# Kernel tuning notes

Hardware: AMD Instinct MI355X
Metric: run time of the kernel (lower is better)

## Reference

```python
import jax, jax.numpy as jnp
import numpy as np
from jax import lax

HEADS = 8
EPS = 1e-5


def _ln2d(x, g, b):
    # LayerNorm over channel axis of BCHW (torch LayerNorm(dim) after b c h w -> b h w c)
    mu = jnp.mean(x, axis=1, keepdims=True)
    var = jnp.mean(jnp.square(x - mu), axis=1, keepdims=True)
    xn = (x - mu) * lax.rsqrt(var + EPS)
    return xn * g[None, :, None, None] + b[None, :, None, None]


def _conv1x1(x, w, b):
    # w: [out_c, in_c]
    return jnp.einsum('bchw,oc->bohw', x, w) + b[None, :, None, None]


def _dwconv3x3(x, w, b):
    # w: [C, 1, 3, 3], depthwise
    y = lax.conv_general_dilated(x, w, window_strides=(1, 1), padding='SAME',
                                 feature_group_count=x.shape[1],
                                 dimension_numbers=('NCHW', 'OIHW', 'NCHW'))
    return y + b[None, :, None, None]


def _gelu(x):
    return jax.nn.gelu(x, approximate=False)


def _linear_attention(x, qkv_w, qkv_b, out_w, out_b):
    B, C, H, W = x.shape
    hd = C // HEADS
    qkv = _conv1x1(x, qkv_w, qkv_b)              # [B, 3C, H, W]
    q, k, v = jnp.split(qkv, 3, axis=1)
    # b (h c) h0 w0 -> b h c (h0 w0)
    q = q.reshape(B, HEADS, hd, H * W)
    k = k.reshape(B, HEADS, hd, H * W)
    v = v.reshape(B, HEADS, hd, H * W)
    q = jax.nn.softmax(q, axis=2)                # over head_dim
    k = jax.nn.softmax(k, axis=3)                # over pixels
    context = jnp.einsum('bhcn,bhdn->bhcd', k, v)  # [B, H, hd, hd]
    out = jnp.einsum('bhcd,bhcn->bhdn', context, q)  # [B, H, hd, N]
    out = out.reshape(B, C, H, W)
    return _conv1x1(out, out_w, out_b)


def _ffn(x, w1, b1, dw_w, dw_b, w2, b2):
    h = _gelu(_conv1x1(x, w1, b1))
    h = _gelu(_dwconv3x3(h, dw_w, dw_b))
    return _conv1x1(h, w2, b2)


def setup_inputs() -> dict:
    key = jax.random.key(0)
    ks = jax.random.split(key, 6)
    B, C, H, W = 4, 192, 256, 256
    hidden = C * 2
    s = 0.02
    return {
        'x': jax.random.normal(ks[0], (B, C, H, W), jnp.float32),
        'ln1_g': jnp.ones((C,), jnp.float32),
        'ln1_b': jnp.zeros((C,), jnp.float32),
        'qkv_w': jax.random.normal(ks[1], (3 * C, C), jnp.float32) * s,
        'qkv_b': jnp.zeros((3 * C,), jnp.float32),
        'out_w': jax.random.normal(ks[2], (C, C), jnp.float32) * s,
        'out_b': jnp.zeros((C,), jnp.float32),
        'ln2_g': jnp.ones((C,), jnp.float32),
        'ln2_b': jnp.zeros((C,), jnp.float32),
        'w1': jax.random.normal(ks[3], (hidden, C), jnp.float32) * s,
        'b1': jnp.zeros((hidden,), jnp.float32),
        'dw_w': jax.random.normal(ks[4], (hidden, 1, 3, 3), jnp.float32) * s,
        'dw_b': jnp.zeros((hidden,), jnp.float32),
        'w2': jax.random.normal(ks[5], (C, hidden), jnp.float32) * s,
        'b2': jnp.zeros((C,), jnp.float32),
    }


def reference(x, ln1_g, ln1_b, qkv_w, qkv_b, out_w, out_b, ln2_g, ln2_b, w1, b1, dw_w, dw_b, w2, b2):
    x = x + _linear_attention(_ln2d(x, ln1_g, ln1_b), qkv_w, qkv_b, out_w, out_b)
    x = x + _ffn(_ln2d(x, ln2_g, ln2_b), w1, b1, dw_w, dw_b, w2, b2)
    return x
```

## Files before the change

kernel.cpp:

```cpp
#include <hip/hip_runtime.h>
#include <math.h>

typedef __attribute__((ext_vector_type(8))) short s8;
typedef __attribute__((ext_vector_type(8))) unsigned short us8;
typedef __attribute__((ext_vector_type(4))) float f4;
typedef __attribute__((ext_vector_type(4))) unsigned short us4;
typedef __attribute__((ext_vector_type(4))) unsigned int u32x4;

#define DEVI __device__ __forceinline__

static const int NPIX = 65536;

DEVI float b2f(unsigned short u) {
    unsigned int v = ((unsigned int)u) << 16;
    float f; __builtin_memcpy(&f, &v, 4); return f;
}
DEVI unsigned short f2b(float f) {
    unsigned int u; __builtin_memcpy(&u, &f, 4);
    unsigned int r = (u + 0x7FFFu + ((u >> 16) & 1u)) >> 16;
    return (unsigned short)r;
}
DEVI float geluf(float x) { return 0.5f * x * (1.0f + erff(x * 0.70710678118f)); }
DEVI float gelu_t(float x) {
    float z = 1.595769122f * (x + 0.044715f * x * x * x);
    return x * __builtin_amdgcn_rcpf(1.0f + __expf(-z));
}
DEVI float rfl(float v) {
    int i; __builtin_memcpy(&i, &v, 4);
    i = __builtin_amdgcn_readfirstlane(i);
    float o; __builtin_memcpy(&o, &i, 4); return o;
}

DEVI void gload_lds16(const unsigned short* g, unsigned short* l) {
    __builtin_amdgcn_global_load_lds(
        (const __attribute__((address_space(1))) unsigned int*)g,
        (__attribute__((address_space(3))) unsigned int*)l,
        16, 0, 0);
}

__global__ __launch_bounds__(256) void lnt_k(const float* __restrict__ X,
                                             const float* __restrict__ gw,
                                             const float* __restrict__ gb,
                                             unsigned short* __restrict__ Out)
{
    const int i = blockIdx.x * 256 + threadIdx.x;
    const int b = i >> 16, px = i & 65535;
    const float* xp = X + (size_t)b * 192 * NPIX + px;

    unsigned int pk[96];
    float sum = 0.f, ssq = 0.f;
    #pragma unroll
    for (int c = 0; c < 192; c++) {
        float v = xp[(size_t)c * NPIX];
        sum += v; ssq += v * v;
        unsigned int h = f2b(v);
        if (c & 1) pk[c >> 1] |= h << 16;
        else       pk[c >> 1] = h;
    }
    float mu = sum * (1.0f / 192.0f);
    float var = ssq * (1.0f / 192.0f) - mu * mu;
    float rs = rsqrtf(var + 1e-5f);

    #pragma unroll
    for (int c2 = 0; c2 < 96; c2++) {
        int c = c2 * 2;
        float lo = b2f((unsigned short)(pk[c2] & 0xFFFF));
        float hi = b2f((unsigned short)(pk[c2] >> 16));
        lo = (lo - mu) * rs * gw[c] + gb[c];
        hi = (hi - mu) * rs * gw[c + 1] + gb[c + 1];
        pk[c2] = (unsigned int)f2b(lo) | ((unsigned int)f2b(hi) << 16);
    }
    u32x4* dst = (u32x4*)(Out + (size_t)i * 192);
    #pragma unroll
    for (int j = 0; j < 6; j++) {
        u32x4 v = { pk[4 * j], pk[4 * j + 1], pk[4 * j + 2], pk[4 * j + 3] };
        dst[j] = v;
    }
}

template<int MODE, int NCHUNK, int UNITS, int NTILE>
__global__ __launch_bounds__(256) void gemm3_k(
    const unsigned short* __restrict__ X, const unsigned short* __restrict__ Wb,
    const float* __restrict__ bias, const void* __restrict__ resid,
    void* __restrict__ Out, int OCTOT, unsigned short* __restrict__ qT)
{
    constexpr int KTOT = UNITS * 192;
    __shared__ unsigned short tile[2][64 * 192];

    const int tid = threadIdx.x;
    const int wave = tid >> 6, lane = tid & 63;
    const int lr = lane & 15, lg = lane >> 4;
    const int xr = lr & 7;

    auto stage = [&](int s, int buf) {
        const int t = s / UNITS, u = s - t * UNITS;
        const int gp0s = (blockIdx.x * NTILE + t) * 64;
        const unsigned short* Xb = X + (size_t)gp0s * KTOT + u * 192;
        #pragma unroll
        for (int j = 0; j < 6; j++) {
            int ci = (wave * 6 + j) * 64 + lane;
            int row = ci / 24;
            int c = ci - row * 24;
            int csw = (c & ~7) | ((c ^ row) & 7);
            gload_lds16(Xb + (size_t)row * KTOT + csw * 8, &tile[buf][ci * 8]);
        }
    };

    stage(0, 0);

    for (int t = 0; t < NTILE; t++) {
        const int gp0 = (blockIdx.x * NTILE + t) * 64;
        const int b = gp0 >> 16;
        const int pxb = gp0 & 65535;

        if constexpr (UNITS == 1) {
            __syncthreads();
            if (t + 1 < NTILE) stage(t + 1, (t + 1) & 1);
            const unsigned short* tb = tile[t & 1];

            #pragma unroll
            for (int cn = 0; cn < NCHUNK; cn++) {
                const int ocb = cn * 192 + wave * 48;
                const unsigned short* wrow = Wb + (size_t)(ocb + lr) * KTOT + lg * 8;
                const bool swapped = (MODE == 1) || (MODE == 3 && cn == 0);

                s8 wf[3][6];
                #pragma unroll
                for (int ot = 0; ot < 3; ot++)
                    #pragma unroll
                    for (int kk = 0; kk < 6; kk++)
                        wf[ot][kk] = *(const s8*)(wrow + (size_t)ot * 16 * KTOT + kk * 32);

                f4 acc[4][3];
                #pragma unroll
                for (int i = 0; i < 4; i++)
                    #pragma unroll
                    for (int j = 0; j < 3; j++) acc[i][j] = (f4)0.0f;

                #pragma unroll
                for (int kk = 0; kk < 6; kk++) {
                    const int kc = kk * 4 + lg;
                    const int kcs = (kc & ~7) | ((kc ^ xr) & 7);
                    s8 a[4];
                    #pragma unroll
                    for (int pt = 0; pt < 4; pt++)
                        a[pt] = *(const s8*)&tb[((pt * 16 + lr) * 24 + kcs) * 8];
                    #pragma unroll
                    for (int ot = 0; ot < 3; ot++)
                        #pragma unroll
                        for (int pt = 0; pt < 4; pt++)
                            acc[pt][ot] = swapped
                                ? __builtin_amdgcn_mfma_f32_16x16x32_bf16(wf[ot][kk], a[pt], acc[pt][ot], 0, 0, 0)
                                : __builtin_amdgcn_mfma_f32_16x16x32_bf16(a[pt], wf[ot][kk], acc[pt][ot], 0, 0, 0);
                }

                if (MODE == 3 && cn == 0) {
                    #pragma unroll
                    for (int pt = 0; pt < 4; pt++) {
                        const int gp = gp0 + pt * 16 + lr;
                        unsigned short* orow = qT + (size_t)gp * 192 + wave * 48 + lg * 4;
                        #pragma unroll
                        for (int ot = 0; ot < 3; ot++) {
                            f4 bi4 = *(const f4*)&bias[wave * 48 + ot * 16 + lg * 4];
                            us4 o;
                            #pragma unroll
                            for (int r = 0; r < 4; r++) o[r] = f2b(__expf(acc[pt][ot][r] + bi4[r]));
                            *(us4*)(orow + ot * 16) = o;
                        }
                    }
                } else if (MODE == 3) {
                    #pragma unroll
                    for (int ot = 0; ot < 3; ot++) {
                        const int oc = ocb + ot * 16 + lr;
                        const float bi = bias[oc];
                        const size_t rowoff = ((size_t)b * 384 + (oc - 192)) * NPIX + pxb + lg * 4;
                        #pragma unroll
                        for (int pt = 0; pt < 4; pt++) {
                            us4 o;
                            #pragma unroll
                            for (int r = 0; r < 4; r++) {
                                float v = acc[pt][ot][r] + bi;
                                if (cn == 1) v = __expf(v);
                                o[r] = f2b(v);
                            }
                            *(us4*)((unsigned short*)Out + rowoff + pt * 16) = o;
                        }
                    }
                } else {
                    #pragma unroll
                    for (int pt = 0; pt < 4; pt++) {
                        const int gp = gp0 + pt * 16 + lr;
                        unsigned short* orow = (unsigned short*)Out + (size_t)gp * OCTOT + ocb + lg * 4;
                        #pragma unroll
                        for (int ot = 0; ot < 3; ot++) {
                            f4 bi4 = *(const f4*)&bias[ocb + ot * 16 + lg * 4];
                            us4 o;
                            #pragma unroll
                            for (int r = 0; r < 4; r++) o[r] = f2b(geluf(acc[pt][ot][r] + bi4[r]));
                            *(us4*)(orow + ot * 16) = o;
                        }
                    }
                }
            }
        } else {
            const int ocb = wave * 48;
            const unsigned short* wrow = Wb + (size_t)(ocb + lr) * KTOT + lg * 8;

            f4 acc[4][3];
            #pragma unroll
            for (int i = 0; i < 4; i++)
                #pragma unroll
                for (int j = 0; j < 3; j++) acc[i][j] = (f4)0.0f;

            #pragma unroll
            for (int u = 0; u < 2; u++) {
                const int s = t * 2 + u;
                __syncthreads();
                if (s + 1 < NTILE * 2) stage(s + 1, (s + 1) & 1);
                const unsigned short* tb = tile[s & 1];

                s8 wf[3][6];
                #pragma unroll
                for (int ot = 0; ot < 3; ot++)
                    #pragma unroll
                    for (int kk = 0; kk < 6; kk++)
                        wf[ot][kk] = *(const s8*)(wrow + (size_t)ot * 16 * KTOT + u * 192 + kk * 32);

                #pragma unroll
                for (int kk = 0; kk < 6; kk++) {
                    const int kc = kk * 4 + lg;
                    const int kcs = (kc & ~7) | ((kc ^ xr) & 7);
                    s8 a[4];
                    #pragma unroll
                    for (int pt = 0; pt < 4; pt++)
                        a[pt] = *(const s8*)&tb[((pt * 16 + lr) * 24 + kcs) * 8];
                    #pragma unroll
                    for (int ot = 0; ot < 3; ot++)
                        #pragma unroll
                        for (int pt = 0; pt < 4; pt++)
                            acc[pt][ot] = __builtin_amdgcn_mfma_f32_16x16x32_bf16(a[pt], wf[ot][kk], acc[pt][ot], 0, 0, 0);
                }
            }

            #pragma unroll
            for (int ot = 0; ot < 3; ot++) {
                const int oc = ocb + ot * 16 + lr;
                const float bi = bias[oc];
                const size_t rowoff = ((size_t)b * 192 + oc) * NPIX + pxb + lg * 4;
                #pragma unroll
                for (int pt = 0; pt < 4; pt++) {
                    if (MODE == 2) {
                        f4 rv = *(const f4*)((const float*)resid + rowoff + pt * 16);
                        f4 o;
                        #pragma unroll
                        for (int r = 0; r < 4; r++) o[r] = acc[pt][ot][r] + bi + rv[r];
                        *(f4*)((float*)Out + rowoff + pt * 16) = o;
                    } else {
                        us4 rv = *(const us4*)((const unsigned short*)resid + rowoff + pt * 16);
                        f4 o;
                        #pragma unroll
                        for (int r = 0; r < 4; r++) o[r] = acc[pt][ot][r] + bi + b2f(rv[r]);
                        *(f4*)((float*)Out + rowoff + pt * 16) = o;
                    }
                }
            }
        }
    }
}

__global__ void zero_k(float* __restrict__ p, int n)
{
    int i = blockIdx.x * 256 + threadIdx.x;
    if (i < n) p[i] = 0.f;
}

__global__ void cvt_k(const float* __restrict__ src, unsigned short* __restrict__ dst, int n)
{
    int i = blockIdx.x * 256 + threadIdx.x;
    if (i < n) dst[i] = f2b(src[i]);
}

__global__ __launch_bounds__(256) void context_k(const unsigned short* __restrict__ kv,
                                                 float* __restrict__ ctxT)
{
    __shared__ float red[4][64][16];
    int bid = blockIdx.x;
    int bh = bid >> 4, cgrp = bid & 15;
    int b = bh >> 3, h = bh & 7;
    int tid = threadIdx.x;
    int wave = tid >> 6, lane = tid & 63, lr = lane & 15, lg = lane >> 4;
    int chunk = cgrp * 4 + wave;
    size_t nbase = (size_t)chunk * 1024 + lg * 8;

    int c0 = h * 24 + lr;
    int c1 = h * 24 + 16 + lr;
    bool val1 = lr < 8;

    const unsigned short* k0p = kv + ((size_t)b * 384 + c0) * NPIX + nbase;
    const unsigned short* k1p = kv + ((size_t)b * 384 + (c1 > 191 ? 191 : c1)) * NPIX + nbase;
    const unsigned short* v0p = kv + ((size_t)b * 384 + 192 + h * 24 + lr) * NPIX + nbase;
    const unsigned short* v1p = kv + ((size_t)b * 384 + 192 + ((h * 24 + 16 + lr > 191) ? 191 : h * 24 + 16 + lr)) * NPIX + nbase;

    const short one_bf = (short)0x3F80;
    s8 ones8 = { one_bf, one_bf, one_bf, one_bf, one_bf, one_bf, one_bf, one_bf };
    s8 zero8 = (s8)0;

    f4 acc[2][2];
    #pragma unroll
    for (int i = 0; i < 2; i++) for (int j = 0; j < 2; j++) acc[i][j] = (f4)0.0f;

    for (int s = 0; s < 32; s++) {
        int off = s * 32;
        s8 p0 = *(const s8*)(k0p + off);
        s8 p1 = *(const s8*)(k1p + off);
        s8 vr0 = *(const s8*)(v0p + off);
        s8 vr1 = *(const s8*)(v1p + off);
        if (!val1) p1 = zero8;
        if (lr == 8) vr1 = ones8;
        acc[0][0] = __builtin_amdgcn_mfma_f32_16x16x32_bf16(p0, vr0, acc[0][0], 0, 0, 0);
        acc[0][1] = __builtin_amdgcn_mfma_f32_16x16x32_bf16(p0, vr1, acc[0][1], 0, 0, 0);
        acc[1][0] = __builtin_amdgcn_mfma_f32_16x16x32_bf16(p1, vr0, acc[1][0], 0, 0, 0);
        acc[1][1] = __builtin_amdgcn_mfma_f32_16x16x32_bf16(p1, vr1, acc[1][1], 0, 0, 0);
    }
    #pragma unroll
    for (int mt = 0; mt < 2; mt++)
        #pragma unroll
        for (int ct = 0; ct < 2; ct++)
            #pragma unroll
            for (int r = 0; r < 4; r++)
                red[wave][lane][mt * 8 + ct * 4 + r] = acc[mt][ct][r];
    __syncthreads();

    if (wave == 0) {
        float* base = ctxT + (size_t)(b * 8 + h) * 1024;
        #pragma unroll
        for (int j = 0; j < 16; j++) {
            float sum = red[0][lane][j] + red[1][lane][j] + red[2][lane][j] + red[3][lane][j];
            int mt = j >> 3, ct = (j >> 2) & 1, r = j & 3;
            int c = mt * 16 + lg * 4 + r;
            int d = ct * 16 + lr;
            atomicAdd(base + d * 32 + c, sum);
        }
    }
}

__global__ void ctxnorm_k(float* __restrict__ ctxT)
{
    int i = blockIdx.x * 256 + threadIdx.x;
    if (i >= 1024) return;
    int bh = i >> 5, c = i & 31;
    float* base = ctxT + (size_t)bh * 1024;
    float den = base[24 * 32 + c];
    float r = den > 0.f ? 1.0f / den : 0.0f;
    #pragma unroll
    for (int d = 0; d < 24; d++) base[d * 32 + c] *= r;
}

template<bool BIGWS>
__global__ __launch_bounds__(256) void qctx_proj_k(
    const unsigned short* __restrict__ qT, const float* __restrict__ ctxT,
    const unsigned short* __restrict__ outWb, const float* __restrict__ outBias,
    const float* __restrict__ xres, float* __restrict__ Out,
    unsigned short* __restrict__ x2b,
    const float* __restrict__ ln2g, const float* __restrict__ ln2b,
    unsigned short* __restrict__ xnt)
{
    __shared__ unsigned short outp[64][200];
    __shared__ float lnS[4][64], lnQ[4][64];

    int tid = threadIdx.x, bid = blockIdx.x;
    int b = bid >> 10, n0 = (bid & 1023) * 64;
    int wave = tid >> 6, lane = tid & 63, lr = lane & 15, lg = lane >> 4;
    const size_t bpx = (size_t)b << 16;

    #pragma unroll
    for (int hh = 0; hh < 2; hh++) {
        int h = wave * 2 + hh;
        s8 cf[2];
        #pragma unroll
        for (int mt = 0; mt < 2; mt++) {
            const float* cp = ctxT + ((size_t)(b * 8 + h) * 32 + mt * 16 + lr) * 32 + lg * 8;
            s8 a;
            #pragma unroll
            for (int j = 0; j < 8; j++) a[j] = (short)f2b(cp[j]);
            cf[mt] = a;
        }
        #pragma unroll
        for (int nt = 0; nt < 4; nt++) {
            int n = nt * 16 + lr;
            s8 bfq = (s8)0;
            float sown = 0.f;
            if (lg < 3) {
                bfq = *(const s8*)(qT + (bpx + n0 + n) * 192 + h * 24 + lg * 8);
                #pragma unroll
                for (int j = 0; j < 8; j++) sown += b2f((unsigned short)bfq[j]);
            }
            float den = sown;
            den += __shfl_xor(den, 16);
            den += __shfl_xor(den, 32);
            f4 z = (f4)0.0f;
            f4 d0 = __builtin_amdgcn_mfma_f32_16x16x32_bf16(cf[0], bfq, z, 0, 0, 0);
            f4 d1 = __builtin_amdgcn_mfma_f32_16x16x32_bf16(cf[1], bfq, z, 0, 0, 0);
            float sinv = 1.0f / den;
            us4 w0;
            #pragma unroll
            for (int r = 0; r < 4; r++) w0[r] = f2b(d0[r] * sinv);
            *(us4*)&outp[n][h * 24 + lg * 4] = w0;
            if (lg < 2) {
                us4 w1;
                #pragma unroll
                for (int r = 0; r < 4; r++) w1[r] = f2b(d1[r] * sinv);
                *(us4*)&outp[n][h * 24 + 16 + lg * 4] = w1;
            }
        }
    }
    __syncthreads();

    f4 acc[4][3];
    #pragma unroll
    for (int i = 0; i < 4; i++) for (int j = 0; j < 3; j++) acc[i][j] = (f4)0.0f;
    #pragma unroll
    for (int k0 = 0; k0 < 192; k0 += 32) {
        s8 bf[4];
        #pragma unroll
        for (int pt = 0; pt < 4; pt++)
            bf[pt] = *(const s8*)&outp[pt * 16 + lr][k0 + lg * 8];
        #pragma unroll
        for (int ot = 0; ot < 3; ot++) {
            s8 af = *(const s8*)&outWb[(size_t)(wave * 48 + ot * 16 + lr) * 192 + k0 + lg * 8];
            #pragma unroll
            for (int pt = 0; pt < 4; pt++)
                acc[pt][ot] = __builtin_amdgcn_mfma_f32_16x16x32_bf16(bf[pt], af, acc[pt][ot], 0, 0, 0);
        }
    }

    float sP[4][4], qP[4][4];
    #pragma unroll
    for (int pt = 0; pt < 4; pt++)
        #pragma unroll
        for (int r = 0; r < 4; r++) { sP[pt][r] = 0.f; qP[pt][r] = 0.f; }

    #pragma unroll
    for (int ot = 0; ot < 3; ot++) {
        const int oc = wave * 48 + ot * 16 + lr;
        const float bi = outBias[oc];
        const size_t rowbase = ((size_t)b * 192 + oc) * NPIX + n0 + lg * 4;
        #pragma unroll
        for (int pt = 0; pt < 4; pt++) {
            f4 rv = *(const f4*)(xres + rowbase + pt * 16);
            f4 v;
            #pragma unroll
            for (int r = 0; r < 4; r++) {
                v[r] = acc[pt][ot][r] + bi + rv[r];
                sP[pt][r] += v[r]; qP[pt][r] += v[r] * v[r];
            }
            acc[pt][ot] = v;
            if (BIGWS) {
                us4 o;
                #pragma unroll
                for (int r = 0; r < 4; r++) o[r] = f2b(v[r]);
                *(us4*)(x2b + rowbase + pt * 16) = o;
            } else {
                *(f4*)(Out + rowbase + pt * 16) = v;
            }
        }
    }
    #pragma unroll
    for (int pt = 0; pt < 4; pt++)
        #pragma unroll
        for (int r = 0; r < 4; r++) {
            float s = sP[pt][r], q = qP[pt][r];
            s += __shfl_xor(s, 1); s += __shfl_xor(s, 2);
            s += __shfl_xor(s, 4); s += __shfl_xor(s, 8);
            q += __shfl_xor(q, 1); q += __shfl_xor(q, 2);
            q += __shfl_xor(q, 4); q += __shfl_xor(q, 8);
            sP[pt][r] = s; qP[pt][r] = q;
        }
    if (lr == 0) {
        #pragma unroll
        for (int pt = 0; pt < 4; pt++)
            #pragma unroll
            for (int r = 0; r < 4; r++) {
                lnS[wave][pt * 16 + lg * 4 + r] = sP[pt][r];
                lnQ[wave][pt * 16 + lg * 4 + r] = qP[pt][r];
            }
    }
    __syncthreads();

    float lgv[3], lbv[3];
    #pragma unroll
    for (int ot = 0; ot < 3; ot++) {
        int oc = wave * 48 + ot * 16 + lr;
        lgv[ot] = ln2g[oc]; lbv[ot] = ln2b[oc];
    }
    #pragma unroll
    for (int pt = 0; pt < 4; pt++) {
        float mu4[4], rs4[4];
        #pragma unroll
        for (int r = 0; r < 4; r++) {
            int px = pt * 16 + lg * 4 + r;
            float S = lnS[0][px] + lnS[1][px] + lnS[2][px] + lnS[3][px];
            float Qq = lnQ[0][px] + lnQ[1][px] + lnQ[2][px] + lnQ[3][px];
            float mu = S * (1.0f / 192.0f);
            float var = Qq * (1.0f / 192.0f) - mu * mu;
            mu4[r] = mu; rs4[r] = rsqrtf(var + 1e-5f);
        }
        #pragma unroll
        for (int ot = 0; ot < 3; ot++) {
            int oc = wave * 48 + ot * 16 + lr;
            #pragma unroll
            for (int r = 0; r < 4; r++) {
                int px = pt * 16 + lg * 4 + r;
                float xn = (acc[pt][ot][r] - mu4[r]) * rs4[r] * lgv[ot] + lbv[ot];
                outp[px][oc] = f2b(xn);
            }
        }
    }
    __syncthreads();

    #pragma unroll
    for (int q = 0; q < 6; q++) {
        int idx = q * 256 + tid;
        int px = idx / 24, c8 = idx % 24;
        us8 v = *(const us8*)&outp[px][c8 * 8];
        *(us8*)(xnt + (bpx + n0 + px) * 192 + c8 * 8) = v;
    }
}

__global__ __launch_bounds__(256) void dwconv_t2_k(
    const unsigned short* __restrict__ h1t, const float* __restrict__ w,
    const float* __restrict__ bias, unsigned short* __restrict__ h2t)
{
    __shared__ unsigned short ring[4 * 4 * 66 * 8];
    const int bz = blockIdx.z;
    const int b = bz / 12, cb = (bz % 12) * 32;
    const int y0 = blockIdx.y * 16, x0 = blockIdx.x * 64;
    const int tid = threadIdx.x;
    const int x = tid & 63, cg = tid >> 6;
    const int c0 = cb + cg * 8;
    const size_t bbase = (size_t)b << 16;

    float wr[9][8], bi[8];
    #pragma unroll
    for (int i = 0; i < 8; i++) {
        #pragma unroll
        for (int j = 0; j < 9; j++) wr[j][i] = rfl(w[(c0 + i) * 9 + j]);
        bi[i] = rfl(bias[c0 + i]);
    }

    const us8 zz = {0, 0, 0, 0, 0, 0, 0, 0};

    auto stage_row = [&](int gy, int s) {
        unsigned short* ldsrow = &ring[((s * 4 + cg) * 66) * 8];
        if (gy >= 0 && gy <= 255) {
            us8 ev = zz;
            if (x == 0 && x0 > 0)
                ev = *(const us8*)(h1t + (bbase + gy * 256 + x0 - 1) * 384 + c0);
            if (x == 63 && x0 + 64 < 256)
                ev = *(const us8*)(h1t + (bbase + gy * 256 + x0 + 64) * 384 + c0);
            gload_lds16(h1t + (bbase + gy * 256 + x0 + x) * 384 + c0,
                        ldsrow + (1 + x) * 8);
            if (x == 0)  *(us8*)&ldsrow[0]      = ev;
            if (x == 63) *(us8*)&ldsrow[65 * 8] = ev;
        } else {
            *(us8*)&ldsrow[(1 + x) * 8] = zz;
            if (x == 0)  *(us8*)&ldsrow[0]      = zz;
            if (x == 63) *(us8*)&ldsrow[65 * 8] = zz;
        }
    };

    stage_row(y0 - 1, 0);
    stage_row(y0,     1);
    stage_row(y0 + 1, 2);
    __syncthreads();

    #pragma unroll
    for (int y = 0; y < 16; y++) {
        if (y < 15) stage_row(y0 + y + 2, (y + 3) & 3);

        float a[8];
        #pragma unroll
        for (int i = 0; i < 8; i++) a[i] = bi[i];
        #pragma unroll
        for (int t = 0; t < 3; t++) {
            const int s = (y + t) & 3;
            const unsigned short* rp = &ring[((s * 4 + cg) * 66 + x) * 8];
            us8 L = *(const us8*)(rp);
            us8 C = *(const us8*)(rp + 8);
            us8 R = *(const us8*)(rp + 16);
            #pragma unroll
            for (int i = 0; i < 8; i++) {
                a[i] += wr[t * 3 + 0][i] * b2f(L[i]);
                a[i] += wr[t * 3 + 1][i] * b2f(C[i]);
                a[i] += wr[t * 3 + 2][i] * b2f(R[i]);
            }
        }
        us8 ov;
        #pragma unroll
        for (int i = 0; i < 8; i++) ov[i] = f2b(gelu_t(a[i]));
        *(us8*)(h2t + (bbase + (y0 + y) * 256 + x0 + x) * 384 + c0) = ov;

        __syncthreads();
    }
}

extern "C" void kernel_launch(void* const* d_in, const int* in_sizes, int n_in,
                              void* d_out, int out_size, void* d_ws, size_t ws_size,
                              hipStream_t stream)
{
    const float* x    = (const float*)d_in[0];
    const float* ln1g = (const float*)d_in[1];
    const float* ln1b = (const float*)d_in[2];
    const float* qkvw = (const float*)d_in[3];
    const float* qkvb = (const float*)d_in[4];
    const float* outw = (const float*)d_in[5];
    const float* outb = (const float*)d_in[6];
    const float* ln2g = (const float*)d_in[7];
    const float* ln2b = (const float*)d_in[8];
    const float* w1   = (const float*)d_in[9];
    const float* b1   = (const float*)d_in[10];
    const float* dww  = (const float*)d_in[11];
    const float* dwb  = (const float*)d_in[12];
    const float* w2   = (const float*)d_in[13];
    const float* b2   = (const float*)d_in[14];
    float* out = (float*)d_out;

    char* ws = (char*)d_ws;
    unsigned short* kv  = (unsigned short*)ws;
    unsigned short* h1t = (unsigned short*)ws;
    unsigned short* h2t = (unsigned short*)(ws + (size_t)201326592);
    unsigned short* qT  = (unsigned short*)(ws + (size_t)201326592);
    unsigned short* xnt = (unsigned short*)(ws + (size_t)301989888);
    size_t off = (size_t)402653184;
    float* koff = (float*)(ws + off); off += 4096;
    float* ctxT = (float*)(ws + off); off += 131072;
    unsigned short* qkvwb = (unsigned short*)(ws + off); off += 221184;
    unsigned short* outwb = (unsigned short*)(ws + off); off += 73728 * 2;
    unsigned short* w1b   = (unsigned short*)(ws + off); off += 147456;
    unsigned short* w2b   = (unsigned short*)(ws + off); off += 147456;
    off = (off + 255) & ~(size_t)255;
    unsigned short* x2b = (unsigned short*)(ws + off);
    const bool bigws = ws_size >= off + (size_t)100663296;
    (void)koff;

    cvt_k<<<(110592 + 255) / 256, 256, 0, stream>>>(qkvw, qkvwb, 110592);
    cvt_k<<<(36864 + 255) / 256, 256, 0, stream>>>(outw, outwb, 36864);
    cvt_k<<<(73728 + 255) / 256, 256, 0, stream>>>(w1, w1b, 73728);
    cvt_k<<<(73728 + 255) / 256, 256, 0, stream>>>(w2, w2b, 73728);

    lnt_k<<<1024, 256, 0, stream>>>(x, ln1g, ln1b, xnt);

    gemm3_k<3, 3, 1, 4><<<1024, 256, 0, stream>>>(xnt, qkvwb, qkvb, nullptr, kv, 384, qT);

    zero_k<<<128, 256, 0, stream>>>(ctxT, 32768);
    context_k<<<512, 256, 0, stream>>>(kv, ctxT);

    ctxnorm_k<<<4, 256, 0, stream>>>(ctxT);

    if (bigws)
        qctx_proj_k<true><<<4096, 256, 0, stream>>>(qT, ctxT, outwb, outb, x, out,
                                                    x2b, ln2g, ln2b, xnt);
    else
        qctx_proj_k<false><<<4096, 256, 0, stream>>>(qT, ctxT, outwb, outb, x, out,
                                                     x2b, ln2g, ln2b, xnt);

    gemm3_k<1, 2, 1, 4><<<1024, 256, 0, stream>>>(xnt, w1b, b1, nullptr, h1t, 384, nullptr);

    dwconv_t2_k<<<dim3(4, 16, 48), 256, 0, stream>>>(h1t, dww, dwb, h2t);

    if (bigws)
        gemm3_k<4, 1, 2, 4><<<1024, 256, 0, stream>>>(h2t, w2b, b2, x2b, out, 192, nullptr);
    else
        gemm3_k<2, 1, 2, 4><<<1024, 256, 0, stream>>>(h2t, w2b, b2, out, out, 192, nullptr);
}
```

Baseline: 895.7 us.

## Fuse FFN first 1x1 conv with GELU into attention-projection kernel

The qctx_proj kernel no longer writes the LayerNorm-2 output (xnt) to global memory. It keeps the normalized tile in shared memory and immediately runs the w1 GEMM with MFMA, applying GELU and storing h1t directly. The separate gemm3_k launch for w1 and its MODE 1 path are removed. This avoids a round trip of a 192-channel bf16 activation through HBM and one kernel launch, at the cost of more registers and work per block in the fused kernel, which may lower occupancy.

```diff
diff --git a/kernel.cpp b/kernel.cpp
--- a/kernel.cpp
+++ b/kernel.cpp
@@ -122,7 +122,7 @@
             for (int cn = 0; cn < NCHUNK; cn++) {
                 const int ocb = cn * 192 + wave * 48;
                 const unsigned short* wrow = Wb + (size_t)(ocb + lr) * KTOT + lg * 8;
-                const bool swapped = (MODE == 1) || (MODE == 3 && cn == 0);
+                const bool swapped = (MODE == 3 && cn == 0);
 
                 s8 wf[3][6];
                 #pragma unroll
@@ -186,20 +186,6 @@
                             *(us4*)((unsigned short*)Out + rowoff + pt * 16) = o;
                         }
                     }
-                } else {
-                    #pragma unroll
-                    for (int pt = 0; pt < 4; pt++) {
-                        const int gp = gp0 + pt * 16 + lr;
-                        unsigned short* orow = (unsigned short*)Out + (size_t)gp * OCTOT + ocb + lg * 4;
-                        #pragma unroll
-                        for (int ot = 0; ot < 3; ot++) {
-                            f4 bi4 = *(const f4*)&bias[ocb + ot * 16 + lg * 4];
-                            us4 o;
-                            #pragma unroll
-                            for (int r = 0; r < 4; r++) o[r] = f2b(geluf(acc[pt][ot][r] + bi4[r]));
-                            *(us4*)(orow + ot * 16) = o;
-                        }
-                    }
                 }
             }
         } else {
@@ -363,7 +349,8 @@
     const float* __restrict__ xres, float* __restrict__ Out,
     unsigned short* __restrict__ x2b,
     const float* __restrict__ ln2g, const float* __restrict__ ln2b,
-    unsigned short* __restrict__ xnt)
+    const unsigned short* __restrict__ w1b, const float* __restrict__ b1,
+    unsigned short* __restrict__ h1t)
 {
     __shared__ unsigned short outp[64][200];
     __shared__ float lnS[4][64], lnQ[4][64];
@@ -519,11 +506,49 @@
     __syncthreads();
 
     #pragma unroll
-    for (int q = 0; q < 6; q++) {
-        int idx = q * 256 + tid;
-        int px = idx / 24, c8 = idx % 24;
-        us8 v = *(const us8*)&outp[px][c8 * 8];
-        *(us8*)(xnt + (bpx + n0 + px) * 192 + c8 * 8) = v;
+    for (int cn = 0; cn < 2; cn++) {
+        const int ocb = cn * 192 + wave * 48;
+        const unsigned short* wrow = w1b + (size_t)(ocb + lr) * 192 + lg * 8;
+
+        s8 wf[3][6];
+        #pragma unroll
+        for (int ot = 0; ot < 3; ot++)
+            #pragma unroll
+            for (int kk = 0; kk < 6; kk++)
+                wf[ot][kk] = *(const s8*)(wrow + (size_t)ot * 16 * 192 + kk * 32);
+
+        f4 acc2[4][3];
+        #pragma unroll
+        for (int i = 0; i < 4; i++)
+            #pragma unroll
+            for (int j = 0; j < 3; j++) acc2[i][j] = (f4)0.0f;
+
+        #pragma unroll
+        for (int kk = 0; kk < 6; kk++) {
+            s8 bf[4];
+            #pragma unroll
+            for (int pt = 0; pt < 4; pt++)
+                bf[pt] = *(const s8*)&outp[pt * 16 + lr][kk * 32 + lg * 8];
+            #pragma unroll
+            for (int ot = 0; ot < 3; ot++)
+                #pragma unroll
+                for (int pt = 0; pt < 4; pt++)
+                    acc2[pt][ot] = __builtin_amdgcn_mfma_f32_16x16x32_bf16(wf[ot][kk], bf[pt], acc2[pt][ot], 0, 0, 0);
+        }
+
+        #pragma unroll
+        for (int pt = 0; pt < 4; pt++) {
+            const int gp = (int)(bpx >> 16) * 0 + n0 + pt * 16 + lr;
+            unsigned short* orow = h1t + (bpx + gp) * 384 + ocb + lg * 4;
+            #pragma unroll
+            for (int ot = 0; ot < 3; ot++) {
+                f4 bi4 = *(const f4*)&b1[ocb + ot * 16 + lg * 4];
+                us4 o;
+                #pragma unroll
+                for (int r = 0; r < 4; r++) o[r] = f2b(geluf(acc2[pt][ot][r] + bi4[r]));
+                *(us4*)(orow + ot * 16) = o;
+            }
+        }
     }
 }
 
@@ -659,12 +684,10 @@
 
     if (bigws)
         qctx_proj_k<true><<<4096, 256, 0, stream>>>(qT, ctxT, outwb, outb, x, out,
-                                                    x2b, ln2g, ln2b, xnt);
+                                                    x2b, ln2g, ln2b, w1b, b1, h1t);
     else
         qctx_proj_k<false><<<4096, 256, 0, stream>>>(qT, ctxT, outwb, outb, x, out,
-                                                     x2b, ln2g, ln2b, xnt);
-
-    gemm3_k<1, 2, 1, 4><<<1024, 256, 0, stream>>>(xnt, w1b, b1, nullptr, h1t, 384, nullptr);
+                                                     x2b, ln2g, ln2b, w1b, b1, h1t);
 
     dwconv_t2_k<<<dim3(4, 16, 48), 256, 0, stream>>>(h1t, dww, dwb, h2t);
 
```

After: 858.6 us. 1.04x faster.
